# Kernel optimization log

Hardware: AMD Instinct MI355X
Metric: run time of the kernel (lower is better)

## Reference

```python
import jax, jax.numpy as jnp
import numpy as np

D_MODEL = 1024
N_HEADS = 16
D_K = D_MODEL // N_HEADS

def _xavier(key, shape):
    fan_in, fan_out = shape[1], shape[0]
    limit = float(np.sqrt(6.0 / (fan_in + fan_out)))
    return jax.random.uniform(key, shape, jnp.float32, -limit, limit)

def setup_inputs() -> dict:
    key = jax.random.key(0)
    ks = jax.random.split(key, 7)
    B, S = 2, 2048
    return {
        "query": jax.random.normal(ks[0], (B, S, D_MODEL), jnp.float32),
        "key": jax.random.normal(ks[1], (B, S, D_MODEL), jnp.float32),
        "value": jax.random.normal(ks[2], (B, S, D_MODEL), jnp.float32),
        "w_q": _xavier(ks[3], (D_MODEL, D_MODEL)),  # torch Linear weight [out, in]
        "w_k": _xavier(ks[4], (D_MODEL, D_MODEL)),
        "w_v": _xavier(ks[5], (D_MODEL, D_MODEL)),
        "w_o": _xavier(ks[6], (D_MODEL, D_MODEL)),
        "ln_gamma": jnp.ones((D_MODEL,), jnp.float32),
        "ln_beta": jnp.zeros((D_MODEL,), jnp.float32),
    }

def reference(query, key, value, w_q, w_k, w_v, w_o, ln_gamma, ln_beta):
    B, S, _ = query.shape
    # projections (torch Linear: x @ W.T), split into heads -> [B, H, S, d_k]
    def split_heads(x, W):
        return (x @ W.T).reshape(B, S, N_HEADS, D_K).transpose(0, 2, 1, 3)
    Q = split_heads(query, w_q)
    K = split_heads(key, w_k)
    V = split_heads(value, w_v)
    scores = jnp.einsum('bhqd,bhkd->bhqk', Q, K) / jnp.sqrt(jnp.float32(D_K))
    attn = jax.nn.softmax(scores, axis=-1)  # dropout disabled (p=0 / eval)
    ctx = jnp.einsum('bhqk,bhkd->bhqd', attn, V)
    ctx = ctx.transpose(0, 2, 1, 3).reshape(B, S, D_MODEL)
    out = ctx @ w_o.T
    # residual + LayerNorm
    x = query + out
    mu = jnp.mean(x, axis=-1, keepdims=True)
    var = jnp.var(x, axis=-1, keepdims=True)
    return (x - mu) / jnp.sqrt(var + 1e-5) * ln_gamma + ln_beta
```

## Files before the change

kernel.cpp:

```cpp
#include <hip/hip_runtime.h>
#include <hip/hip_bf16.h>

#define DEVI __device__ __forceinline__

typedef float f32x4 __attribute__((ext_vector_type(4)));
typedef short bf16x8 __attribute__((ext_vector_type(8)));
typedef unsigned short ushort_t;

DEVI ushort_t f2bf(float x) {
  union { float f; unsigned u; } c; c.f = x;
  unsigned u = c.u;
  unsigned r = (u + 0x7fffu + ((u >> 16) & 1u)) >> 16;
  return (ushort_t)r;
}

DEVI float bf2f(unsigned hw) {
  union { unsigned u; float f; } c; c.u = hw << 16; return c.f;
}

DEVI unsigned cvt_pk_bf16(float lo, float hi) {
  unsigned r;
  asm volatile("v_cvt_pk_bf16_f32 %0, %1, %2" : "=v"(r) : "v"(lo), "v"(hi));
  return r;
}

DEVI void gload16(const ushort_t* g, ushort_t* l) {
  __builtin_amdgcn_global_load_lds(
      (const __attribute__((address_space(1))) unsigned int*)g,
      (__attribute__((address_space(3))) unsigned int*)l, 16, 0, 0);
}


__global__ __launch_bounds__(256)
void cvt_all_kernel(const float* __restrict__ p0, const float* __restrict__ p1,
                    const float* __restrict__ p2,
                    const float* __restrict__ w0, const float* __restrict__ w1,
                    const float* __restrict__ w2, const float* __restrict__ w3,
                    ushort_t* __restrict__ o0, ushort_t* __restrict__ o1,
                    ushort_t* __restrict__ o2,
                    ushort_t* __restrict__ q0, ushort_t* __restrict__ q1,
                    ushort_t* __restrict__ q2, ushort_t* __restrict__ q3) {
  int z = blockIdx.y;
  int i = blockIdx.x * 256 + threadIdx.x;
  const float* in;
  ushort_t* out;
  if (z < 3) {
    in = (z == 0) ? p0 : (z == 1) ? p1 : p2;
    out = (z == 0) ? o0 : (z == 1) ? o1 : o2;
  } else {
    int w = i >> 17;
    int local = i & 131071;
    in = ((w == 0) ? w0 : (w == 1) ? w1 : (w == 2) ? w2 : w3);
    out = ((w == 0) ? q0 : (w == 1) ? q1 : (w == 2) ? q2 : q3);
    i = local;
  }
  const float4* p = (const float4*)in + (size_t)i * 2;
  float4 a = p[0], b = p[1];
  uint4 v;
  v.x = cvt_pk_bf16(a.x, a.y);
  v.y = cvt_pk_bf16(a.z, a.w);
  v.z = cvt_pk_bf16(b.x, b.y);
  v.w = cvt_pk_bf16(b.z, b.w);
  ((uint4*)out)[i] = v;
}


__global__ __launch_bounds__(256)
void gemm128(const ushort_t* __restrict__ A0, const ushort_t* __restrict__ A1,
             const ushort_t* __restrict__ A2,
             const ushort_t* __restrict__ W0, const ushort_t* __restrict__ W1,
             const ushort_t* __restrict__ W2,
             void* __restrict__ O0, void* __restrict__ O1,
             void* __restrict__ O2, int mode_base, int nsteps, float qscale) {
  constexpr int K = 1024;
  int z = blockIdx.z;
  int mode = (mode_base == 3) ? 3 : mode_base + z;
  const ushort_t* A = (z == 0) ? A0 : (z == 1) ? A1 : A2;
  const ushort_t* W = (z == 0) ? W0 : (z == 1) ? W1 : W2;
  void* Op = (z == 0) ? O0 : (z == 1) ? O1 : O2;
  if (mode == 3) {
    A = A0 + z * 512;
    W = W0 + z * 512;
    Op = z ? O1 : O0;
  }
  float scale = (mode == 0) ? qscale : 1.0f;
  int m0 = (mode == 2) ? blockIdx.y * 128 : blockIdx.x * 128;
  int n0 = (mode == 2) ? blockIdx.x * 128 : blockIdx.y * 128;

  __shared__ __align__(16) ushort_t Asm[128 * 64];
  __shared__ __align__(16) ushort_t Bsm[128 * 64];

  int t = threadIdx.x;
  int lane = t & 63, wave = t >> 6;
  int wm = wave >> 1, wn = wave & 1;
  int col = lane & 15, g = lane >> 4;
  int lr = lane >> 3, lc = lane & 7;
  int cswz = col & 7;

  const ushort_t* aSrc = A + (size_t)(m0 + wave * 32 + lr) * K + (lc ^ lr) * 8;
  const ushort_t* bSrc = W + (size_t)(n0 + wave * 32 + lr) * K + (lc ^ lr) * 8;

  f32x4 z4 = {0.f, 0.f, 0.f, 0.f};
  f32x4 acc[4][4];
  for (int i = 0; i < 4; i++)
    for (int j = 0; j < 4; j++) acc[i][j] = z4;

  for (int kt = 0; kt < nsteps; ++kt) {
    int koff = kt * 64;
#pragma unroll
    for (int i_ = 0; i_ < 4; i_++) {
      gload16(aSrc + koff + i_ * 8 * K, &Asm[(wave * 32 + i_ * 8) * 64]);
      gload16(bSrc + koff + i_ * 8 * K, &Bsm[(wave * 32 + i_ * 8) * 64]);
    }
    __syncthreads();
#pragma unroll
    for (int kk = 0; kk < 2; ++kk) {
      bf16x8 af[4], bfr[4];
#pragma unroll
      for (int mi = 0; mi < 4; mi++) {
        int row = wm * 64 + mi * 16 + col;
        af[mi] = *(const bf16x8*)(Asm + row * 64 + (((kk * 4 + g) ^ cswz) * 8));
      }
#pragma unroll
      for (int ni = 0; ni < 4; ni++) {
        int row = wn * 64 + ni * 16 + col;
        bfr[ni] = *(const bf16x8*)(Bsm + row * 64 + (((kk * 4 + g) ^ cswz) * 8));
      }
      __builtin_amdgcn_s_setprio(1);
#pragma unroll
      for (int mi = 0; mi < 4; mi++)
#pragma unroll
        for (int ni = 0; ni < 4; ni++)
          acc[mi][ni] = __builtin_amdgcn_mfma_f32_16x16x32_bf16(af[mi], bfr[ni],
                                                                acc[mi][ni], 0, 0, 0);
      __builtin_amdgcn_s_setprio(0);
    }
    __syncthreads();
  }

#pragma unroll
  for (int mi = 0; mi < 4; mi++)
#pragma unroll
    for (int ni = 0; ni < 4; ni++)
#pragma unroll
      for (int r = 0; r < 4; r++) {
        int m = m0 + wm * 64 + mi * 16 + g * 4 + r;
        int n = n0 + wn * 64 + ni * 16 + col;
        float v = acc[mi][ni][r] * scale;
        if (mode <= 1) {
          int b = m >> 11, s = m & 2047, h = n >> 6, d = n & 63;
          ((ushort_t*)Op)[(((size_t)(b * 16 + h) * 2048 + s) * 64) + d] = f2bf(v);
        } else if (mode == 2) {
          int h = m >> 6, d = m & 63, b = n >> 11, s = n & 2047;
          ((ushort_t*)Op)[(((size_t)(b * 16 + h) * 64 + d) * 2048) + s] = f2bf(v);
        } else {
          ((ushort_t*)Op)[(size_t)m * 1024 + n] = f2bf(v);
        }
      }
}


__global__ __launch_bounds__(256, 4)
void attn_kernel(const ushort_t* __restrict__ Qh, const ushort_t* __restrict__ Kh,
                 const ushort_t* __restrict__ Vt,
                 ushort_t* __restrict__ op0, ushort_t* __restrict__ op1,
                 float* __restrict__ lp0, float* __restrict__ lp1) {
  int bh = blockIdx.x;
  int qt = blockIdx.y;
  int sp = blockIdx.z;
  int t = threadIdx.x, lane = t & 63, wave = t >> 6;
  int col = lane & 15, g = lane >> 4;
  int lr = lane >> 3, lc = lane & 7;
  int cswz = col & 7;
  int q0 = qt * 128 + wave * 32;
  int kbase = sp * 1024;
  ushort_t* opart = sp ? op1 : op0;
  float* lpart = sp ? lp1 : lp0;

  const ushort_t* Qp = Qh + (size_t)bh * 2048 * 64;
  const ushort_t* Kp = Kh + (size_t)bh * 2048 * 64;
  const ushort_t* Vp = Vt + (size_t)bh * 64 * 2048;

  __shared__ __align__(16) ushort_t Ksm[2][64 * 64];
  __shared__ __align__(16) ushort_t Vsm[2][64 * 64];

  int slot0 = wave * 16 + lr;
  int slot1 = slot0 + 8;
  int key0 = (slot0 & 0x20) | ((slot0 & 0x0C) << 1) | ((slot0 & 0x10) >> 2) | (slot0 & 3);
  int key1 = (slot1 & 0x20) | ((slot1 & 0x0C) << 1) | ((slot1 & 0x10) >> 2) | (slot1 & 3);

  const ushort_t* kSrc0 = Kp + (size_t)key0 * 64 + (lc ^ lr) * 8;
  const ushort_t* kSrc1 = Kp + (size_t)key1 * 64 + (lc ^ lr) * 8;
  const ushort_t* vSrc = Vp + (size_t)(wave * 16 + lr) * 2048 + (lc ^ lr) * 8;

#define ATTN_STAGE(buf, k0) do { \
    gload16(kSrc0 + (size_t)(k0) * 64, &Ksm[buf][wave * 1024]);        \
    gload16(kSrc1 + (size_t)(k0) * 64, &Ksm[buf][wave * 1024 + 512]);  \
    gload16(vSrc + (k0),               &Vsm[buf][wave * 1024]);        \
    gload16(vSrc + (k0) + 16384,       &Vsm[buf][wave * 1024 + 512]);  \
  } while (0)

  bf16x8 qa0 = *(const bf16x8*)(Qp + (size_t)(q0 + col) * 64 + g * 8);
  bf16x8 qa1 = *(const bf16x8*)(Qp + (size_t)(q0 + col) * 64 + 32 + g * 8);
  bf16x8 qb0 = *(const bf16x8*)(Qp + (size_t)(q0 + 16 + col) * 64 + g * 8);
  bf16x8 qb1 = *(const bf16x8*)(Qp + (size_t)(q0 + 16 + col) * 64 + 32 + g * 8);

  f32x4 z4 = {0.f, 0.f, 0.f, 0.f};
  f32x4 oa[4], ob[4];
  for (int i = 0; i < 4; i++) { oa[i] = z4; ob[i] = z4; }
  f32x4 la = z4, lb = z4;

  ATTN_STAGE(0, kbase);
  __syncthreads();

  for (int it = 0; it < 16; ++it) {
    int cur = it & 1;
    int k0 = kbase + it * 64;
    if (it < 15) ATTN_STAGE(cur ^ 1, k0 + 64);

    const ushort_t* Ks = Ksm[cur];
    const ushort_t* Vs = Vsm[cur];

    f32x4 sa[4], sb[4];
#pragma unroll
    for (int kt = 0; kt < 4; kt++) {
      int off = (kt * 16 + col) * 64 + ((g ^ cswz) * 8);
      bf16x8 kf0 = *(const bf16x8*)(Ks + off);
      bf16x8 kf1 = *(const bf16x8*)(Ks + (off ^ 32));
      f32x4 a = z4, b = z4;
      __builtin_amdgcn_s_setprio(1);
      a = __builtin_amdgcn_mfma_f32_16x16x32_bf16(kf0, qa0, a, 0, 0, 0);
      a = __builtin_amdgcn_mfma_f32_16x16x32_bf16(kf1, qa1, a, 0, 0, 0);
      b = __builtin_amdgcn_mfma_f32_16x16x32_bf16(kf0, qb0, b, 0, 0, 0);
      b = __builtin_amdgcn_mfma_f32_16x16x32_bf16(kf1, qb1, b, 0, 0, 0);
      __builtin_amdgcn_s_setprio(0);
      sa[kt] = a; sb[kt] = b;
    }

    unsigned pka[8], pkb[8];
#pragma unroll
    for (int kt = 0; kt < 4; kt++) {
      float a0 = __builtin_amdgcn_exp2f(sa[kt][0]);
      float a1 = __builtin_amdgcn_exp2f(sa[kt][1]);
      float a2 = __builtin_amdgcn_exp2f(sa[kt][2]);
      float a3 = __builtin_amdgcn_exp2f(sa[kt][3]);
      la[0] += a0; la[1] += a1; la[2] += a2; la[3] += a3;
      pka[2 * kt]     = cvt_pk_bf16(a0, a1);
      pka[2 * kt + 1] = cvt_pk_bf16(a2, a3);
      float b0 = __builtin_amdgcn_exp2f(sb[kt][0]);
      float b1 = __builtin_amdgcn_exp2f(sb[kt][1]);
      float b2 = __builtin_amdgcn_exp2f(sb[kt][2]);
      float b3 = __builtin_amdgcn_exp2f(sb[kt][3]);
      lb[0] += b0; lb[1] += b1; lb[2] += b2; lb[3] += b3;
      pkb[2 * kt]     = cvt_pk_bf16(b0, b1);
      pkb[2 * kt + 1] = cvt_pk_bf16(b2, b3);
    }

#pragma unroll
    for (int kk = 0; kk < 2; kk++) {
      union { uint4 u; bf16x8 f; } ua, ub;
      ua.u.x = pka[4 * kk];     ua.u.y = pka[4 * kk + 1];
      ua.u.z = pka[4 * kk + 2]; ua.u.w = pka[4 * kk + 3];
      ub.u.x = pkb[4 * kk];     ub.u.y = pkb[4 * kk + 1];
      ub.u.z = pkb[4 * kk + 2]; ub.u.w = pkb[4 * kk + 3];
      __builtin_amdgcn_s_setprio(1);
#pragma unroll
      for (int dt = 0; dt < 4; dt++) {
        bf16x8 vf = *(const bf16x8*)(Vs + (dt * 16 + col) * 64 +
                                     (((kk * 4 + g) ^ cswz) * 8));
        oa[dt] = __builtin_amdgcn_mfma_f32_16x16x32_bf16(vf, ua.f, oa[dt], 0, 0, 0);
        ob[dt] = __builtin_amdgcn_mfma_f32_16x16x32_bf16(vf, ub.f, ob[dt], 0, 0, 0);
      }
      __builtin_amdgcn_s_setprio(0);
    }
    __syncthreads();
  }
#undef ATTN_STAGE

  float lva = (la[0] + la[1]) + (la[2] + la[3]);
  lva += __shfl_xor(lva, 16);
  lva += __shfl_xor(lva, 32);
  float lvb = (lb[0] + lb[1]) + (lb[2] + lb[3]);
  lvb += __shfl_xor(lvb, 16);
  lvb += __shfl_xor(lvb, 32);
  if (g == 0) {
    lpart[(size_t)bh * 2048 + q0 + col] = lva;
    lpart[(size_t)bh * 2048 + q0 + 16 + col] = lvb;
  }
  int b = bh >> 4, h = bh & 15;
#pragma unroll
  for (int dt = 0; dt < 4; dt++)
#pragma unroll
    for (int rp = 0; rp < 2; rp++) {
      int d = dt * 16 + g * 4 + rp * 2;
      unsigned pa = cvt_pk_bf16(oa[dt][rp * 2], oa[dt][rp * 2 + 1]);
      unsigned pb = cvt_pk_bf16(ob[dt][rp * 2], ob[dt][rp * 2 + 1]);
      *(unsigned*)(opart + ((size_t)(b * 2048 + q0 + col)) * 1024 + h * 64 + d) = pa;
      *(unsigned*)(opart + ((size_t)(b * 2048 + q0 + 16 + col)) * 1024 + h * 64 + d) = pb;
    }
}


__global__ __launch_bounds__(256)
void attn_reduce(const ushort_t* __restrict__ o0, const ushort_t* __restrict__ o1,
                 const float* __restrict__ l0, const float* __restrict__ l1,
                 ushort_t* __restrict__ ctx) {
  int m = blockIdx.x;
  int t = threadIdx.x;
  int b = m >> 11, q = m & 2047;
  int h = t >> 4;
  size_t li = (size_t)(b * 16 + h) * 2048 + q;
  float inv = 1.0f / (l0[li] + l1[li]);
  uint2 a = ((const uint2*)(o0 + (size_t)m * 1024))[t];
  uint2 c = ((const uint2*)(o1 + (size_t)m * 1024))[t];
  float x0 = (bf2f(a.x & 0xffffu) + bf2f(c.x & 0xffffu)) * inv;
  float x1 = (bf2f(a.x >> 16)     + bf2f(c.x >> 16))     * inv;
  float x2 = (bf2f(a.y & 0xffffu) + bf2f(c.y & 0xffffu)) * inv;
  float x3 = (bf2f(a.y >> 16)     + bf2f(c.y >> 16))     * inv;
  uint2 o;
  o.x = cvt_pk_bf16(x0, x1);
  o.y = cvt_pk_bf16(x2, x3);
  ((uint2*)(ctx + (size_t)m * 1024))[t] = o;
}


__global__ __launch_bounds__(256)
void ln_kernel(const float* __restrict__ resid, const ushort_t* __restrict__ p0,
               const ushort_t* __restrict__ p1,
               const float* __restrict__ gamma, const float* __restrict__ beta,
               float* __restrict__ out) {
  int m = blockIdx.x;
  int t = threadIdx.x;
  int lane = t & 63, wave = t >> 6;
  float4 a = ((const float4*)(resid + (size_t)m * 1024))[t];
  uint2 v0 = ((const uint2*)(p0 + (size_t)m * 1024))[t];
  uint2 v1 = ((const uint2*)(p1 + (size_t)m * 1024))[t];
  float4 x;
  x.x = a.x + bf2f(v0.x & 0xffffu) + bf2f(v1.x & 0xffffu);
  x.y = a.y + bf2f(v0.x >> 16)     + bf2f(v1.x >> 16);
  x.z = a.z + bf2f(v0.y & 0xffffu) + bf2f(v1.y & 0xffffu);
  x.w = a.w + bf2f(v0.y >> 16)     + bf2f(v1.y >> 16);
  float sum = (x.x + x.y) + (x.z + x.w);
  float ssq = x.x * x.x + x.y * x.y + x.z * x.z + x.w * x.w;
  for (int off = 1; off < 64; off <<= 1) {
    sum += __shfl_xor(sum, off);
    ssq += __shfl_xor(ssq, off);
  }
  __shared__ float red[8];
  if (lane == 0) { red[wave] = sum; red[4 + wave] = ssq; }
  __syncthreads();
  sum = red[0] + red[1] + red[2] + red[3];
  ssq = red[4] + red[5] + red[6] + red[7];
  float mu = sum * (1.f / 1024.f);
  float var = ssq * (1.f / 1024.f) - mu * mu;
  float rstd = rsqrtf(var + 1e-5f);
  const float4* gp = (const float4*)gamma;
  const float4* bp = (const float4*)beta;
  float4 gg = gp[t], bb = bp[t];
  float4 y;
  y.x = (x.x - mu) * rstd * gg.x + bb.x;
  y.y = (x.y - mu) * rstd * gg.y + bb.y;
  y.z = (x.z - mu) * rstd * gg.z + bb.z;
  y.w = (x.w - mu) * rstd * gg.w + bb.w;
  ((float4*)(out + (size_t)m * 1024))[t] = y;
}


extern "C" void kernel_launch(void* const* d_in, const int* in_sizes, int n_in,
                              void* d_out, int out_size, void* d_ws, size_t ws_size,
                              hipStream_t stream) {
  (void)in_sizes; (void)n_in; (void)out_size; (void)ws_size;
  const float* query = (const float*)d_in[0];
  const float* keyi  = (const float*)d_in[1];
  const float* value = (const float*)d_in[2];
  const float* w_q = (const float*)d_in[3];
  const float* w_k = (const float*)d_in[4];
  const float* w_v = (const float*)d_in[5];
  const float* w_o = (const float*)d_in[6];
  const float* ln_g = (const float*)d_in[7];
  const float* ln_b = (const float*)d_in[8];

  char* ws = (char*)d_ws;
  const size_t MB = 1u << 20;
  ushort_t* Xq  = (ushort_t*)(ws + 0 * MB);
  ushort_t* Xk  = (ushort_t*)(ws + 8 * MB);
  ushort_t* Xv  = (ushort_t*)(ws + 16 * MB);
  ushort_t* op0 = (ushort_t*)(ws + 0 * MB);
  ushort_t* op1 = (ushort_t*)(ws + 8 * MB);
  float*    l0  = (float*)   (ws + 16 * MB);
  float*    l1  = (float*)   (ws + 17 * MB);
  ushort_t* proj0 = (ushort_t*)(ws + 0 * MB);
  ushort_t* proj1 = (ushort_t*)(ws + 8 * MB);
  ushort_t* Wq  = (ushort_t*)(ws + 24 * MB);
  ushort_t* Wk  = (ushort_t*)(ws + 26 * MB);
  ushort_t* Wv  = (ushort_t*)(ws + 28 * MB);
  ushort_t* Wo  = (ushort_t*)(ws + 30 * MB);
  ushort_t* Qh  = (ushort_t*)(ws + 32 * MB);
  ushort_t* Kh  = (ushort_t*)(ws + 40 * MB);
  ushort_t* Vt  = (ushort_t*)(ws + 48 * MB);
  ushort_t* ctx = (ushort_t*)(ws + 56 * MB);

  const float SCL = 0.18033688f;

  cvt_all_kernel<<<dim3(2048, 4), 256, 0, stream>>>(
      query, keyi, value, w_q, w_k, w_v, w_o,
      Xq, Xk, Xv, Wq, Wk, Wv, Wo);

  gemm128<<<dim3(32, 8, 3), 256, 0, stream>>>(Xq, Xk, Wv, Wq, Wk, Xv,
                                              Qh, Kh, Vt, 0, 16, SCL);
  attn_kernel<<<dim3(32, 16, 2), 256, 0, stream>>>(Qh, Kh, Vt,
                                                   op0, op1, l0, l1);
  attn_reduce<<<4096, 256, 0, stream>>>(op0, op1, l0, l1, ctx);
  gemm128<<<dim3(32, 8, 2), 256, 0, stream>>>(ctx, ctx, ctx, Wo, Wo, Wo,
                                              proj0, proj1, proj0, 3, 8, 1.0f);
  ln_kernel<<<4096, 256, 0, stream>>>(query, proj0, proj1, ln_g, ln_b,
                                      (float*)d_out);
}
```

Measured before the change: 127.9 us.

## Fuse fp32-to-bf16 activation conversion into QKV projection GEMM loads

Drops the separate conversion pass over query/key/value. The projection GEMM now reads fp32 activations directly into registers, converts them to bf16 and writes them to shared memory, prefetching the next k-tile during compute; only the weights are still converted by a smaller kernel. This removes one full fp32 read plus bf16 write-and-reread of the activations, at the cost of doubled global bytes per GEMM tile load and register-staged loads in place of direct global-to-LDS loads. The attention kernel's launch-bounds occupancy hint also drops from 4 to 3 blocks.

New measurement: 123.9 us. 1.03x faster.

```diff
diff --git a/kernel.cpp b/kernel.cpp
--- a/kernel.cpp
+++ b/kernel.cpp
@@ -32,28 +32,14 @@
 
 
 __global__ __launch_bounds__(256)
-void cvt_all_kernel(const float* __restrict__ p0, const float* __restrict__ p1,
-                    const float* __restrict__ p2,
-                    const float* __restrict__ w0, const float* __restrict__ w1,
-                    const float* __restrict__ w2, const float* __restrict__ w3,
-                    ushort_t* __restrict__ o0, ushort_t* __restrict__ o1,
-                    ushort_t* __restrict__ o2,
-                    ushort_t* __restrict__ q0, ushort_t* __restrict__ q1,
-                    ushort_t* __restrict__ q2, ushort_t* __restrict__ q3) {
+void cvt_w_kernel(const float* __restrict__ w0, const float* __restrict__ w1,
+                  const float* __restrict__ w2, const float* __restrict__ w3,
+                  ushort_t* __restrict__ q0, ushort_t* __restrict__ q1,
+                  ushort_t* __restrict__ q2, ushort_t* __restrict__ q3) {
   int z = blockIdx.y;
   int i = blockIdx.x * 256 + threadIdx.x;
-  const float* in;
-  ushort_t* out;
-  if (z < 3) {
-    in = (z == 0) ? p0 : (z == 1) ? p1 : p2;
-    out = (z == 0) ? o0 : (z == 1) ? o1 : o2;
-  } else {
-    int w = i >> 17;
-    int local = i & 131071;
-    in = ((w == 0) ? w0 : (w == 1) ? w1 : (w == 2) ? w2 : w3);
-    out = ((w == 0) ? q0 : (w == 1) ? q1 : (w == 2) ? q2 : q3);
-    i = local;
-  }
+  const float* in = (z == 0) ? w0 : (z == 1) ? w1 : (z == 2) ? w2 : w3;
+  ushort_t* out = (z == 0) ? q0 : (z == 1) ? q1 : (z == 2) ? q2 : q3;
   const float4* p = (const float4*)in + (size_t)i * 2;
   float4 a = p[0], b = p[1];
   uint4 v;
@@ -66,23 +52,24 @@
 
 
 __global__ __launch_bounds__(256)
-void gemm128(const ushort_t* __restrict__ A0, const ushort_t* __restrict__ A1,
-             const ushort_t* __restrict__ A2,
-             const ushort_t* __restrict__ W0, const ushort_t* __restrict__ W1,
-             const ushort_t* __restrict__ W2,
+void gemm128(const void* A0v, const void* A1v, const void* A2v,
+             const void* W0v, const void* W1v, const void* W2v,
              void* __restrict__ O0, void* __restrict__ O1,
              void* __restrict__ O2, int mode_base, int nsteps, float qscale) {
   constexpr int K = 1024;
   int z = blockIdx.z;
   int mode = (mode_base == 3) ? 3 : mode_base + z;
-  const ushort_t* A = (z == 0) ? A0 : (z == 1) ? A1 : A2;
-  const ushort_t* W = (z == 0) ? W0 : (z == 1) ? W1 : W2;
+  const void* Av = (z == 0) ? A0v : (z == 1) ? A1v : A2v;
+  const void* Wv = (z == 0) ? W0v : (z == 1) ? W1v : W2v;
   void* Op = (z == 0) ? O0 : (z == 1) ? O1 : O2;
   if (mode == 3) {
-    A = A0 + z * 512;
-    W = W0 + z * 512;
+    Av = (const ushort_t*)A0v + z * 512;
+    Wv = (const ushort_t*)W0v + z * 512;
     Op = z ? O1 : O0;
   }
+  bool aF32 = (mode <= 1);
+  bool bF32 = (mode == 2);
+  bool fused = aF32 || bF32;
   float scale = (mode == 0) ? qscale : 1.0f;
   int m0 = (mode == 2) ? blockIdx.y * 128 : blockIdx.x * 128;
   int n0 = (mode == 2) ? blockIdx.x * 128 : blockIdx.y * 128;
@@ -97,22 +84,61 @@
   int lr = lane >> 3, lc = lane & 7;
   int cswz = col & 7;
 
-  const ushort_t* aSrc = A + (size_t)(m0 + wave * 32 + lr) * K + (lc ^ lr) * 8;
-  const ushort_t* bSrc = W + (size_t)(n0 + wave * 32 + lr) * K + (lc ^ lr) * 8;
+  int rowA = m0 + wave * 32 + lr;
+  int rowB = n0 + wave * 32 + lr;
+  const ushort_t* aSrcB = (const ushort_t*)Av + (size_t)rowA * K + (lc ^ lr) * 8;
+  const ushort_t* bSrcB = (const ushort_t*)Wv + (size_t)rowB * K + (lc ^ lr) * 8;
+  const float* fSrc = aF32
+      ? ((const float*)Av + (size_t)rowA * K + (lc ^ lr) * 8)
+      : ((const float*)Wv + (size_t)rowB * K + (lc ^ lr) * 8);
+  ushort_t* fDst = aF32 ? Asm : Bsm;
+  int fOffBase = (wave * 32 + lr) * 64 + lc * 8;
 
   f32x4 z4 = {0.f, 0.f, 0.f, 0.f};
   f32x4 acc[4][4];
   for (int i = 0; i < 4; i++)
     for (int j = 0; j < 4; j++) acc[i][j] = z4;
 
+  float4 fr[4][2];
+
+#define FLOAD(koff) do {                                                   \
+    _Pragma("unroll")                                                      \
+    for (int i_ = 0; i_ < 4; i_++) {                                       \
+      const float* p_ = fSrc + (size_t)(i_ * 8) * K + (koff);              \
+      fr[i_][0] = *(const float4*)p_;                                      \
+      fr[i_][1] = *(const float4*)(p_ + 4);                                \
+    }                                                                      \
+  } while (0)
+
+#define FWRITE() do {                                                      \
+    _Pragma("unroll")                                                      \
+    for (int i_ = 0; i_ < 4; i_++) {                                       \
+      uint4 w_;                                                            \
+      w_.x = cvt_pk_bf16(fr[i_][0].x, fr[i_][0].y);                        \
+      w_.y = cvt_pk_bf16(fr[i_][0].z, fr[i_][0].w);                        \
+      w_.z = cvt_pk_bf16(fr[i_][1].x, fr[i_][1].y);                        \
+      w_.w = cvt_pk_bf16(fr[i_][1].z, fr[i_][1].w);                        \
+      *(uint4*)(fDst + fOffBase + i_ * 8 * 64) = w_;                       \
+    }                                                                      \
+  } while (0)
+
+  if (fused) FLOAD(0);
+
   for (int kt = 0; kt < nsteps; ++kt) {
     int koff = kt * 64;
-#pragma unroll
-    for (int i_ = 0; i_ < 4; i_++) {
-      gload16(aSrc + koff + i_ * 8 * K, &Asm[(wave * 32 + i_ * 8) * 64]);
-      gload16(bSrc + koff + i_ * 8 * K, &Bsm[(wave * 32 + i_ * 8) * 64]);
+    if (fused) FWRITE();
+    if (!aF32) {
+#pragma unroll
+      for (int i_ = 0; i_ < 4; i_++)
+        gload16(aSrcB + koff + i_ * 8 * K, &Asm[(wave * 32 + i_ * 8) * 64]);
+    }
+    if (!bF32) {
+#pragma unroll
+      for (int i_ = 0; i_ < 4; i_++)
+        gload16(bSrcB + koff + i_ * 8 * K, &Bsm[(wave * 32 + i_ * 8) * 64]);
     }
     __syncthreads();
+    if (fused && kt + 1 < nsteps) FLOAD(koff + 64);
 #pragma unroll
     for (int kk = 0; kk < 2; ++kk) {
       bf16x8 af[4], bfr[4];
@@ -157,10 +183,12 @@
           ((ushort_t*)Op)[(size_t)m * 1024 + n] = f2bf(v);
         }
       }
-}
-
-
-__global__ __launch_bounds__(256, 4)
+#undef FLOAD
+#undef FWRITE
+}
+
+
+__global__ __launch_bounds__(256, 3)
 void attn_kernel(const ushort_t* __restrict__ Qh, const ushort_t* __restrict__ Kh,
                  const ushort_t* __restrict__ Vt,
                  ushort_t* __restrict__ op0, ushort_t* __restrict__ op1,
@@ -382,9 +410,6 @@
 
   char* ws = (char*)d_ws;
   const size_t MB = 1u << 20;
-  ushort_t* Xq  = (ushort_t*)(ws + 0 * MB);
-  ushort_t* Xk  = (ushort_t*)(ws + 8 * MB);
-  ushort_t* Xv  = (ushort_t*)(ws + 16 * MB);
   ushort_t* op0 = (ushort_t*)(ws + 0 * MB);
   ushort_t* op1 = (ushort_t*)(ws + 8 * MB);
   float*    l0  = (float*)   (ws + 16 * MB);
@@ -402,11 +427,11 @@
 
   const float SCL = 0.18033688f;
 
-  cvt_all_kernel<<<dim3(2048, 4), 256, 0, stream>>>(
-      query, keyi, value, w_q, w_k, w_v, w_o,
-      Xq, Xk, Xv, Wq, Wk, Wv, Wo);
-
-  gemm128<<<dim3(32, 8, 3), 256, 0, stream>>>(Xq, Xk, Wv, Wq, Wk, Xv,
+  cvt_w_kernel<<<dim3(512, 4), 256, 0, stream>>>(w_q, w_k, w_v, w_o,
+                                                 Wq, Wk, Wv, Wo);
+
+  gemm128<<<dim3(32, 8, 3), 256, 0, stream>>>(query, keyi, Wv,
+                                              Wq, Wk, value,
                                               Qh, Kh, Vt, 0, 16, SCL);
   attn_kernel<<<dim3(32, 16, 2), 256, 0, stream>>>(Qh, Kh, Vt,
                                                    op0, op1, l0, l1);
```
